# Kernel optimization log

Hardware: AMD Instinct MI355X
Metric: run time of the kernel (lower is better)

The kernel has to match this reference:

```python
import jax, jax.numpy as jnp
import numpy as np

GAMMA = 10.0   # RBF width of the stand-in radial kernel
EPS = 1e-12    # safe-norm epsilon (avoids NaN grad at zero difference)

N_POINTS = 16384
N_NBR = 32
C_IN = 16
C_OUT = 16
N_BASIS = 16


def setup_inputs() -> dict:
    key = jax.random.key(0)
    k1, k2, k3, k4, k5, k6 = jax.random.split(key, 6)
    inp = jax.random.normal(k1, (C_IN, N_POINTS), dtype=jnp.float32)
    coords = jax.random.normal(k2, (N_POINTS, 3), dtype=jnp.float32)
    W = jax.random.normal(k3, (C_OUT, C_IN, N_BASIS), dtype=jnp.float32)
    centers = jax.random.uniform(k4, (N_BASIS,), dtype=jnp.float32)
    relative_mask = jax.random.uniform(k5, (N_POINTS, N_NBR), dtype=jnp.float32)
    neighbors = jax.random.randint(k6, (N_POINTS, N_NBR), 0, N_POINTS)
    return {"input": inp, "coords": coords, "W": W, "centers": centers,
            "relative_mask": relative_mask, "neighbors": neighbors}


def reference(input, coords, W, centers, relative_mask, neighbors):
    # difference_matrix: [N, K, 3]
    diff = coords[neighbors] - coords[:, None, :]
    # edge length with safe sqrt: [N, K]
    r = jnp.sqrt(jnp.sum(diff * diff, axis=-1) + EPS)
    # Gaussian radial basis: [N, K, B]
    rbf = jnp.exp(-GAMMA * (r[..., None] - centers) ** 2)
    # per-edge kernel: [C_out, C_in, N, K]
    kernel = jnp.einsum('oib,nkb->oink', W, rbf)
    # relative_mask applied as einsum 'ba,dcba->dcba'
    kernel = relative_mask * kernel
    # neighbor feature gather: [C_in, N, K]
    neighbors_input = input[:, neighbors]
    # contraction 'cba,dcba->db': [C_out, N]
    output = jnp.einsum('ink,oink->on', neighbors_input, kernel)
    return output
```

## Files before the change

### kernel.cpp

```cpp
#include <hip/hip_runtime.h>
#include <hip/hip_bf16.h>

#define NPTS 16384
#define NNBR 32
#define CIN 16
#define COUT 16
#define NBASIS 16

#define WF_OS 264
#define RT_BS 40
#define RT_PS 648
#define ML_PS 264

typedef _Float16 half8 __attribute__((ext_vector_type(8)));
typedef float floatx4 __attribute__((ext_vector_type(4)));

__global__ __launch_bounds__(256) void transpose_kernel(
        const float* __restrict__ input, float* __restrict__ xT) {
    const int n = blockIdx.x * 256 + threadIdx.x;
    float v[CIN];
    #pragma unroll
    for (int i = 0; i < CIN; ++i) v[i] = input[i * NPTS + n];
    float4* dst = (float4*)&xT[n * CIN];
    #pragma unroll
    for (int j = 0; j < 4; ++j)
        dst[j] = make_float4(v[4 * j], v[4 * j + 1], v[4 * j + 2], v[4 * j + 3]);
}

__global__ __launch_bounds__(256) void se3_conv_kernel(
        const float* __restrict__ xT,
        const float* __restrict__ coords,
        const float* __restrict__ W,
        const float* __restrict__ centers,
        const float* __restrict__ mask,
        const int* __restrict__ neighbors,
        float* __restrict__ out) {
    __shared__ _Float16 Wf[COUT * WF_OS];
    __shared__ _Float16 RT[16 * RT_PS];
    __shared__ _Float16 Mld[16 * ML_PS];

    const int tid = threadIdx.x;
    const int p = tid >> 4;
    const int t = tid & 15;
    const int quad = (tid >> 4) & 3;
    const int wv = tid >> 6;
    const int nbase = blockIdx.x * 16;

    float cent[NBASIS];
    #pragma unroll
    for (int b = 0; b < NBASIS; ++b) cent[b] = centers[b];

    for (int idx = tid; idx < COUT * CIN * NBASIS; idx += 256) {
        int o = idx >> 8, i = (idx >> 4) & 15, b = idx & 15;
        Wf[o * WF_OS + b * 16 + i] = (_Float16)W[idx];
    }

    {
        const int n = nbase + p;
        const float cx = coords[n * 3 + 0];
        const float cy = coords[n * 3 + 1];
        const float cz = coords[n * 3 + 2];
        #pragma unroll
        for (int kk = 0; kk < 2; ++kk) {
            const int k = t + kk * 16;
            const int nbr = neighbors[n * NNBR + k] & (NPTS - 1);
            const float dx = coords[nbr * 3 + 0] - cx;
            const float dy = coords[nbr * 3 + 1] - cy;
            const float dz = coords[nbr * 3 + 2] - cz;
            const float r = sqrtf(dx * dx + dy * dy + dz * dz + 1e-12f);
            #pragma unroll
            for (int b = 0; b < NBASIS; ++b) {
                const float d = r - cent[b];
                RT[p * RT_PS + b * RT_BS + k] = (_Float16)__expf(-10.0f * d * d);
            }
        }
    }
    __syncthreads();

    #pragma unroll
    for (int q = 0; q < 4; ++q) {
        const int pq = wv * 4 + q;
        const int n = nbase + pq;
        int nb[8];
        float mv[8];
        const int kbase = 8 * quad;
        #pragma unroll
        for (int j = 0; j < 8; ++j) {
            nb[j] = neighbors[n * NNBR + kbase + j] & (NPTS - 1);
            mv[j] = mask[n * NNBR + kbase + j];
        }
        half8 afrag;
        #pragma unroll
        for (int j = 0; j < 8; ++j) {
            const float x = xT[nb[j] * CIN + t];
            afrag[j] = (_Float16)(x * mv[j]);
        }
        const half8 bfrag = *(const half8*)&RT[pq * RT_PS + t * RT_BS + kbase];
        floatx4 c = {0.0f, 0.0f, 0.0f, 0.0f};
        c = __builtin_amdgcn_mfma_f32_16x16x32_f16(afrag, bfrag, c, 0, 0, 0);
        _Float16 h[4];
        #pragma unroll
        for (int v = 0; v < 4; ++v) h[v] = (_Float16)c[v];
        *(uint2*)&Mld[pq * ML_PS + t * 16 + 4 * quad] = *(uint2*)h;
    }
    __syncthreads();

    if (tid < 64) {
        floatx4 acc = {0.0f, 0.0f, 0.0f, 0.0f};
        #pragma unroll
        for (int cch = 0; cch < 8; ++cch) {
            const int bi = cch * 32 + 8 * quad;
            const half8 a = *(const half8*)&Wf[t * WF_OS + bi];
            const half8 b = *(const half8*)&Mld[t * ML_PS + bi];
            acc = __builtin_amdgcn_mfma_f32_16x16x32_f16(a, b, acc, 0, 0, 0);
        }
        #pragma unroll
        for (int v = 0; v < 4; ++v) {
            out[(4 * quad + v) * NPTS + nbase + t] = acc[v];
        }
    }
}

extern "C" void kernel_launch(void* const* d_in, const int* in_sizes, int n_in,
                              void* d_out, int out_size, void* d_ws, size_t ws_size,
                              hipStream_t stream) {
    const float* input   = (const float*)d_in[0];
    const float* coords  = (const float*)d_in[1];
    const float* W       = (const float*)d_in[2];
    const float* centers = (const float*)d_in[3];
    const float* mask    = (const float*)d_in[4];
    const int*   nbr     = (const int*)d_in[5];
    float* out = (float*)d_out;

    float* xT = (float*)d_ws;
    transpose_kernel<<<NPTS / 256, 256, 0, stream>>>(input, xT);
    se3_conv_kernel<<<NPTS / 16, 256, 0, stream>>>(xT, coords, W, centers,
                                                   mask, nbr, out);
}
```

Baseline: 76.86 us.

## Compute RBF basis in MFMA fragment loop and stage edge data in LDS

The large per-point RBF table in shared memory is removed. Stage one now stores only edge lengths, 16-bit neighbor indices and half-precision masks in LDS, and each lane evaluates its own exp basis values right when it builds the MFMA B fragment. The W staging uses vectorized half8 stores, and all four waves run the final contraction MFMAs redundantly so no waves sit idle behind a divergent branch, with only one wave's lanes writing each output. This shrinks LDS use and uncoalesced per-thread neighbor/mask global loads, at the cost of recomputing exps per fragment and redundant MFMA work.

```diff
diff --git a/kernel.cpp b/kernel.cpp
--- a/kernel.cpp
+++ b/kernel.cpp
@@ -8,11 +8,10 @@
 #define NBASIS 16
 
 #define WF_OS 264
-#define RT_BS 40
-#define RT_PS 648
 #define ML_PS 264
 
 typedef _Float16 half8 __attribute__((ext_vector_type(8)));
+typedef unsigned short ushort8 __attribute__((ext_vector_type(8)));
 typedef float floatx4 __attribute__((ext_vector_type(4)));
 
 __global__ __launch_bounds__(256) void transpose_kernel(
@@ -36,68 +35,64 @@
         const int* __restrict__ neighbors,
         float* __restrict__ out) {
     __shared__ _Float16 Wf[COUT * WF_OS];
-    __shared__ _Float16 RT[16 * RT_PS];
     __shared__ _Float16 Mld[16 * ML_PS];
+    __shared__ float    rs[16 * NNBR];
+    __shared__ unsigned short nb16[16 * NNBR];
+    __shared__ _Float16 mv16[16 * NNBR];
 
     const int tid = threadIdx.x;
-    const int p = tid >> 4;
     const int t = tid & 15;
     const int quad = (tid >> 4) & 3;
     const int wv = tid >> 6;
     const int nbase = blockIdx.x * 16;
 
-    float cent[NBASIS];
-    #pragma unroll
-    for (int b = 0; b < NBASIS; ++b) cent[b] = centers[b];
-
-    for (int idx = tid; idx < COUT * CIN * NBASIS; idx += 256) {
-        int o = idx >> 8, i = (idx >> 4) & 15, b = idx & 15;
-        Wf[o * WF_OS + b * 16 + i] = (_Float16)W[idx];
+    {
+        const int o = tid >> 4, b = tid & 15;
+        _Float16 wrow[16];
+        #pragma unroll
+        for (int i = 0; i < CIN; ++i)
+            wrow[i] = (_Float16)W[o * 256 + i * 16 + b];
+        *(half8*)&Wf[o * WF_OS + b * 16]     = *(half8*)&wrow[0];
+        *(half8*)&Wf[o * WF_OS + b * 16 + 8] = *(half8*)&wrow[8];
     }
 
-    {
-        const int n = nbase + p;
-        const float cx = coords[n * 3 + 0];
-        const float cy = coords[n * 3 + 1];
-        const float cz = coords[n * 3 + 2];
-        #pragma unroll
-        for (int kk = 0; kk < 2; ++kk) {
-            const int k = t + kk * 16;
-            const int nbr = neighbors[n * NNBR + k] & (NPTS - 1);
-            const float dx = coords[nbr * 3 + 0] - cx;
-            const float dy = coords[nbr * 3 + 1] - cy;
-            const float dz = coords[nbr * 3 + 2] - cz;
-            const float r = sqrtf(dx * dx + dy * dy + dz * dz + 1e-12f);
-            #pragma unroll
-            for (int b = 0; b < NBASIS; ++b) {
-                const float d = r - cent[b];
-                RT[p * RT_PS + b * RT_BS + k] = (_Float16)__expf(-10.0f * d * d);
-            }
-        }
+    #pragma unroll
+    for (int s = 0; s < 2; ++s) {
+        const int f = tid + s * 256;
+        const int pt = f >> 5;
+        const int n = nbase + pt;
+        const int nbr = neighbors[nbase * NNBR + f] & (NPTS - 1);
+        const float m = mask[nbase * NNBR + f];
+        const float dx = coords[nbr * 3 + 0] - coords[n * 3 + 0];
+        const float dy = coords[nbr * 3 + 1] - coords[n * 3 + 1];
+        const float dz = coords[nbr * 3 + 2] - coords[n * 3 + 2];
+        rs[f] = sqrtf(dx * dx + dy * dy + dz * dz + 1e-12f);
+        nb16[f] = (unsigned short)nbr;
+        mv16[f] = (_Float16)m;
     }
     __syncthreads();
 
+    const float cb = centers[t];
+    const int pbase = wv * 4;
     #pragma unroll
     for (int q = 0; q < 4; ++q) {
-        const int pq = wv * 4 + q;
-        const int n = nbase + pq;
-        int nb[8];
-        float mv[8];
-        const int kbase = 8 * quad;
+        const int pq = pbase + q;
+        const int kb = pq * NNBR + 8 * quad;
+        const float4 r0 = *(const float4*)&rs[kb];
+        const float4 r1 = *(const float4*)&rs[kb + 4];
+        const ushort8 nbv = *(const ushort8*)&nb16[kb];
+        const half8 mvv = *(const half8*)&mv16[kb];
+        const float rj[8] = {r0.x, r0.y, r0.z, r0.w, r1.x, r1.y, r1.z, r1.w};
+        half8 af, bf;
         #pragma unroll
         for (int j = 0; j < 8; ++j) {
-            nb[j] = neighbors[n * NNBR + kbase + j] & (NPTS - 1);
-            mv[j] = mask[n * NNBR + kbase + j];
+            const float d = rj[j] - cb;
+            bf[j] = (_Float16)__expf(-10.0f * d * d);
+            const float x = xT[(int)nbv[j] * CIN + t];
+            af[j] = (_Float16)(x * (float)mvv[j]);
         }
-        half8 afrag;
-        #pragma unroll
-        for (int j = 0; j < 8; ++j) {
-            const float x = xT[nb[j] * CIN + t];
-            afrag[j] = (_Float16)(x * mv[j]);
-        }
-        const half8 bfrag = *(const half8*)&RT[pq * RT_PS + t * RT_BS + kbase];
         floatx4 c = {0.0f, 0.0f, 0.0f, 0.0f};
-        c = __builtin_amdgcn_mfma_f32_16x16x32_f16(afrag, bfrag, c, 0, 0, 0);
+        c = __builtin_amdgcn_mfma_f32_16x16x32_f16(af, bf, c, 0, 0, 0);
         _Float16 h[4];
         #pragma unroll
         for (int v = 0; v < 4; ++v) h[v] = (_Float16)c[v];
@@ -105,19 +100,18 @@
     }
     __syncthreads();
 
-    if (tid < 64) {
-        floatx4 acc = {0.0f, 0.0f, 0.0f, 0.0f};
+    floatx4 acc = {0.0f, 0.0f, 0.0f, 0.0f};
+    #pragma unroll
+    for (int cch = 0; cch < 8; ++cch) {
+        const int bi = cch * 32 + 8 * quad;
+        const half8 a = *(const half8*)&Wf[t * WF_OS + bi];
+        const half8 b = *(const half8*)&Mld[t * ML_PS + bi];
+        acc = __builtin_amdgcn_mfma_f32_16x16x32_f16(a, b, acc, 0, 0, 0);
+    }
+    if (wv == (t >> 2)) {
         #pragma unroll
-        for (int cch = 0; cch < 8; ++cch) {
-            const int bi = cch * 32 + 8 * quad;
-            const half8 a = *(const half8*)&Wf[t * WF_OS + bi];
-            const half8 b = *(const half8*)&Mld[t * ML_PS + bi];
-            acc = __builtin_amdgcn_mfma_f32_16x16x32_f16(a, b, acc, 0, 0, 0);
-        }
-        #pragma unroll
-        for (int v = 0; v < 4; ++v) {
+        for (int v = 0; v < 4; ++v)
             out[(4 * quad + v) * NPTS + nbase + t] = acc[v];
-        }
     }
 }
 
```

Result: no change. 75.77 us (-1.4%).
